# Kernel optimization log

Hardware: AMD Instinct MI355X
Metric: run time of the kernel (lower is better)

## Reference

```python
import jax, jax.numpy as jnp
import numpy as np

FFT_BINS = 513   # win_length//2 + 1
WIN = 1024       # win_length
H = 128          # LSTM hidden size (both blocks)
ENC = 256        # encoder_size
EPS = 1e-7


def _lstm_cell(x, h, c, Wih, Whh, bih, bhh):
    # x: [1, in], h/c: [1, H]; PyTorch gate order i, f, g, o
    g = x @ Wih.T + bih + h @ Whh.T + bhh
    i, f, gg, o = jnp.split(g, 4, axis=-1)
    c2 = jax.nn.sigmoid(f) * c + jax.nn.sigmoid(i) * jnp.tanh(gg)
    h2 = jax.nn.sigmoid(o) * jnp.tanh(c2)
    return h2, c2


def _sep_block(x, states, Wih0, Whh0, bih0, bhh0, Wih1, Whh1, bih1, bhh1, dw, db):
    # x: [1,1,in]; states: [1,1,2*2*H] -> [2(h/c), 2(layers), 1, H]
    st = states.reshape(2, 2, 1, H)
    h0, c0 = st[0], st[1]
    xt = x[:, 0]                                   # [1, in]
    h1, c1 = _lstm_cell(xt, h0[0], c0[0], Wih0, Whh0, bih0, bhh0)
    h2, c2 = _lstm_cell(h1, h0[1], c0[1], Wih1, Whh1, bih1, bhh1)
    mask = jax.nn.sigmoid(h2 @ dw.T + db)[:, None, :]   # [1,1,in]
    out_states = jnp.stack([jnp.stack([h1, h2]), jnp.stack([c1, c2])]).reshape(1, 1, -1)
    return mask, out_states


def setup_inputs() -> dict:
    key = jax.random.key(0)
    ks = jax.random.split(key, 32)
    s = 0.08  # ~ 1/sqrt(H), matching PyTorch LSTM init scale
    def n(i, shape, sc=s):
        return jax.random.normal(ks[i], shape, dtype=jnp.float32) * sc
    inp = {
        "mag": jax.random.uniform(ks[0], (1, 1, FFT_BINS), dtype=jnp.float32),
        "phase": n(1, (1, 1, FFT_BINS), 3.0),
        "in_states1": n(2, (1, 1, 2 * 2 * H), 1.0),
        "in_states2": n(3, (1, 1, 2 * 2 * H), 1.0),
        # sep1 LSTM (input 513)
        "w_ih1_0": n(4, (4 * H, FFT_BINS)), "w_hh1_0": n(5, (4 * H, H)),
        "b_ih1_0": n(6, (4 * H,)), "b_hh1_0": n(7, (4 * H,)),
        "w_ih1_1": n(8, (4 * H, H)), "w_hh1_1": n(9, (4 * H, H)),
        "b_ih1_1": n(10, (4 * H,)), "b_hh1_1": n(11, (4 * H,)),
        "dense1_w": n(12, (FFT_BINS, H)), "dense1_b": n(13, (FFT_BINS,)),
        # encoder 1x1 conv (no bias) + instant layernorm
        "enc_w": n(14, (ENC, WIN)),
        "gamma": jnp.ones((1, 1, ENC), jnp.float32),
        "beta": jnp.zeros((1, 1, ENC), jnp.float32),
        # sep2 LSTM (input 256)
        "w_ih2_0": n(15, (4 * H, ENC)), "w_hh2_0": n(16, (4 * H, H)),
        "b_ih2_0": n(17, (4 * H,)), "b_hh2_0": n(18, (4 * H,)),
        "w_ih2_1": n(19, (4 * H, H)), "w_hh2_1": n(20, (4 * H, H)),
        "b_ih2_1": n(21, (4 * H,)), "b_hh2_1": n(22, (4 * H,)),
        "dense2_w": n(23, (ENC, H)), "dense2_b": n(24, (ENC,)),
        # decoder 1x1 conv (no bias)
        "dec_w": n(25, (WIN, ENC)),
    }
    return inp


def reference(mag, phase, in_states1, in_states2,
              w_ih1_0, w_hh1_0, b_ih1_0, b_hh1_0,
              w_ih1_1, w_hh1_1, b_ih1_1, b_hh1_1,
              dense1_w, dense1_b, enc_w, gamma, beta,
              w_ih2_0, w_hh2_0, b_ih2_0, b_hh2_0,
              w_ih2_1, w_hh2_1, b_ih2_1, b_hh2_1,
              dense2_w, dense2_b, dec_w):
    # Branch 1: magnitude masking in STFT domain
    mask1, out_states1 = _sep_block(mag, in_states1, w_ih1_0, w_hh1_0, b_ih1_0,
                                    b_hh1_0, w_ih1_1, w_hh1_1, b_ih1_1, b_hh1_1,
                                    dense1_w, dense1_b)
    est_mag = mask1 * mag
    s1_stft = est_mag * jnp.exp(1j * phase)          # [1,1,513] complex64
    y1 = jnp.fft.irfft(s1_stft, axis=-1)             # [1,1,1024]
    # encoder 1x1 conv (permute + conv1d(k=1) == matmul over channels)
    enc = jnp.einsum('btw,ew->bte', y1, enc_w)       # [1,1,256]
    # instant layer norm over channels
    mean = jnp.mean(enc, axis=-1, keepdims=True)
    var = jnp.mean(jnp.square(enc - mean), axis=-1, keepdims=True)
    enc_norm = (enc - mean) / jnp.sqrt(var + EPS) * gamma + beta
    # Branch 2: learned-domain masking
    mask2, out_states2 = _sep_block(enc_norm, in_states2, w_ih2_0, w_hh2_0,
                                    b_ih2_0, b_hh2_0, w_ih2_1, w_hh2_1,
                                    b_ih2_1, b_hh2_1, dense2_w, dense2_b)
    est_enc = mask2 * enc
    decoded = jnp.einsum('bte,we->bwt', est_enc, dec_w)  # [1,1024,1]
    return decoded, out_states1, out_states2
```

## Files before the change

### kernel.cpp

```cpp
#include <hip/hip_runtime.h>
#include <hip/hip_bf16.h>


#define HDIM 128
typedef __hip_bfloat16 bf16;

__device__ float G[4608];
#define O_H1A 0
#define O_H2A 128
#define O_C1A 256
#define O_C2A 384
#define O_H1B 512
#define O_H2B 640
#define O_C1B 768
#define O_C2B 896
#define O_XR  1024
#define O_XI  1600
#define O_Y   2176
#define O_ENC 3200
#define O_EST 3456

__device__ __forceinline__ bool is_bf(const void* probe) {
    return (((const unsigned*)probe)[0] & 0xFFFFu) == 0x3F80u;
}
__device__ __forceinline__ float ldin(const void* p, int i, bool bf) {
    return bf ? __bfloat162float(((const bf16*)p)[i]) : ((const float*)p)[i];
}
__device__ __forceinline__ void stout(void* p, int i, float v, bool bf) {
    if (bf) ((bf16*)p)[i] = __float2bfloat16(v);
    else    ((float*)p)[i] = v;
}
__device__ __forceinline__ float wred(float v) {
#pragma unroll
    for (int m = 32; m; m >>= 1) v += __shfl_xor(v, m);
    return v;
}
__device__ __forceinline__ float sigm(float x) { return 1.f / (1.f + expf(-x)); }

template <int LX, bool XINT>
__global__ __launch_bounds__(256) void k_lstm(
    const void* __restrict__ xp, int xoff,
    const void* __restrict__ st, int hoff, int coff,
    const void* __restrict__ Wih, const void* __restrict__ Whh,
    const void* __restrict__ bih, const void* __restrict__ bhh,
    int ho, int co, const void* __restrict__ probe)
{
    const bool bf = is_bf(probe);
    __shared__ float xs[LX];
    __shared__ float hs[HDIM];
    __shared__ float g4[4];
    const int tid = threadIdx.x, lane = tid & 63, wave = tid >> 6;
    const int j = blockIdx.x;
    for (int i = tid; i < LX; i += 256)
        xs[i] = XINT ? G[xoff + i] : ldin(xp, xoff + i, bf);
    for (int i = tid; i < HDIM; i += 256)
        hs[i] = ldin(st, hoff + i, bf);
    __syncthreads();
    const int row = wave * HDIM + j;
    float acc = 0.f;
    for (int k = lane; k < LX; k += 64) acc += ldin(Wih, row * LX + k, bf) * xs[k];
    for (int k = lane; k < HDIM; k += 64) acc += ldin(Whh, row * HDIM + k, bf) * hs[k];
    acc = wred(acc);
    if (lane == 0) g4[wave] = acc + ldin(bih, row, bf) + ldin(bhh, row, bf);
    __syncthreads();
    if (tid == 0) {
        float cin = ldin(st, coff + j, bf);
        float c2 = sigm(g4[1]) * cin + sigm(g4[0]) * tanhf(g4[2]);
        float h2 = sigm(g4[3]) * tanhf(c2);
        G[ho + j] = h2;
        G[co + j] = c2;
    }
}

__global__ __launch_bounds__(256) void k_lstm_ln(
    const void* __restrict__ gamma, const void* __restrict__ beta,
    const void* __restrict__ st,
    const void* __restrict__ Wih, const void* __restrict__ Whh,
    const void* __restrict__ bih, const void* __restrict__ bhh,
    const void* __restrict__ probe)
{
    const bool bf = is_bf(probe);
    __shared__ float xs[256];
    __shared__ float hs[HDIM];
    __shared__ float red[4];
    __shared__ float g4[4];
    const int tid = threadIdx.x, lane = tid & 63, wave = tid >> 6;
    const int j = blockIdx.x;
    float v = G[O_ENC + tid];
    float s = wred(v);
    if (lane == 0) red[wave] = s;
    __syncthreads();
    float mean = (red[0] + red[1] + red[2] + red[3]) * (1.f / 256.f);
    __syncthreads();
    float d = v - mean;
    float s2 = wred(d * d);
    if (lane == 0) red[wave] = s2;
    __syncthreads();
    float var = (red[0] + red[1] + red[2] + red[3]) * (1.f / 256.f);
    float rs = rsqrtf(var + 1e-7f);
    xs[tid] = d * rs * ldin(gamma, tid, bf) + ldin(beta, tid, bf);
    for (int i = tid; i < HDIM; i += 256) hs[i] = ldin(st, i, bf);
    __syncthreads();
    const int row = wave * HDIM + j;
    float acc = 0.f;
    for (int k = lane; k < 256; k += 64) acc += ldin(Wih, row * 256 + k, bf) * xs[k];
    for (int k = lane; k < HDIM; k += 64) acc += ldin(Whh, row * HDIM + k, bf) * hs[k];
    acc = wred(acc);
    if (lane == 0) g4[wave] = acc + ldin(bih, row, bf) + ldin(bhh, row, bf);
    __syncthreads();
    if (tid == 0) {
        float cin = ldin(st, 256 + j, bf);
        float c2 = sigm(g4[1]) * cin + sigm(g4[0]) * tanhf(g4[2]);
        float h2 = sigm(g4[3]) * tanhf(c2);
        G[O_H1B + j] = h2;
        G[O_C1B + j] = c2;
    }
}

__global__ __launch_bounds__(256) void k_mask1(
    const void* __restrict__ dw, const void* __restrict__ db,
    const void* __restrict__ mag, const void* __restrict__ phase,
    void* __restrict__ out, const void* __restrict__ probe)
{
    const bool bf = is_bf(probe);
    __shared__ float hs[HDIM];
    const int tid = threadIdx.x, lane = tid & 63, wave = tid >> 6;
    for (int i = tid; i < HDIM; i += 256) hs[i] = G[O_H2A + i];
    __syncthreads();
    const int g = blockIdx.x * 4 + wave;
    if (g < 513) {
        float acc = 0.f;
        for (int k = lane; k < HDIM; k += 64) acc += ldin(dw, g * HDIM + k, bf) * hs[k];
        acc = wred(acc);
        if (lane == 0) {
            float m = sigm(acc + ldin(db, g, bf));
            float em = m * ldin(mag, g, bf);
            float p = ldin(phase, g, bf);
            float sp, cp;
            sincosf(p, &sp, &cp);
            G[O_XR + g] = em * cp;
            G[O_XI + g] = em * sp;
        }
    }
    if (blockIdx.x == 0) {
        for (int t = tid; t < 512; t += 256) stout(out, 1024 + t, G[t], bf);
    }
}

__global__ __launch_bounds__(256) void k_irfft()
{
    __shared__ float xr[513], xi[513];
    const int tid = threadIdx.x, lane = tid & 63, wave = tid >> 6;
    for (int i = tid; i < 513; i += 256) { xr[i] = G[O_XR + i]; xi[i] = G[O_XI + i]; }
    __syncthreads();
    const int n = blockIdx.x * 4 + wave;
    float acc = 0.f;
    for (int k = lane; k < 513; k += 64) {
        if (k == 0) {
            acc += xr[0];
        } else if (k == 512) {
            acc += (n & 1) ? -xr[512] : xr[512];
        } else {
            int m = (k * n) & 1023;
            float th = (float)m * (6.283185307179586f / 1024.f);
            float sn, cs;
            sincosf(th, &sn, &cs);
            acc += 2.f * (xr[k] * cs - xi[k] * sn);
        }
    }
    acc = wred(acc);
    if (lane == 0) G[O_Y + n] = acc * (1.f / 1024.f);
}

__global__ __launch_bounds__(256) void k_enc(
    const void* __restrict__ ew, const void* __restrict__ probe)
{
    const bool bf = is_bf(probe);
    __shared__ float ys[1024];
    const int tid = threadIdx.x, lane = tid & 63, wave = tid >> 6;
    for (int i = tid; i < 1024; i += 256) ys[i] = G[O_Y + i];
    __syncthreads();
    const int e = blockIdx.x * 4 + wave;
    float acc = 0.f;
    for (int k = lane; k < 1024; k += 64) acc += ldin(ew, e * 1024 + k, bf) * ys[k];
    acc = wred(acc);
    if (lane == 0) G[O_ENC + e] = acc;
}

__global__ __launch_bounds__(256) void k_mask2(
    const void* __restrict__ dw, const void* __restrict__ db,
    void* __restrict__ out, const void* __restrict__ probe)
{
    const bool bf = is_bf(probe);
    __shared__ float hs[HDIM];
    const int tid = threadIdx.x, lane = tid & 63, wave = tid >> 6;
    for (int i = tid; i < HDIM; i += 256) hs[i] = G[O_H2B + i];
    __syncthreads();
    const int e = blockIdx.x * 4 + wave;
    float acc = 0.f;
    for (int k = lane; k < HDIM; k += 64) acc += ldin(dw, e * HDIM + k, bf) * hs[k];
    acc = wred(acc);
    if (lane == 0) {
        float m = sigm(acc + ldin(db, e, bf));
        G[O_EST + e] = m * G[O_ENC + e];
    }
    if (blockIdx.x == 0) {
        for (int t = tid; t < 512; t += 256) stout(out, 1536 + t, G[512 + t], bf);
    }
}

__global__ __launch_bounds__(256) void k_dec(
    const void* __restrict__ dw, void* __restrict__ out, const void* __restrict__ probe)
{
    const bool bf = is_bf(probe);
    __shared__ float es[256];
    const int tid = threadIdx.x, lane = tid & 63, wave = tid >> 6;
    es[tid] = G[O_EST + tid];
    __syncthreads();
    const int w = blockIdx.x * 4 + wave;
    float acc = 0.f;
    for (int k = lane; k < 256; k += 64) acc += ldin(dw, w * 256 + k, bf) * es[k];
    acc = wred(acc);
    if (lane == 0) stout(out, w, acc, bf);
}

extern "C" void kernel_launch(void* const* d_in, const int* in_sizes, int n_in,
                              void* d_out, int out_size, void* d_ws, size_t ws_size,
                              hipStream_t stream)
{
    const void* mag      = d_in[0];
    const void* phase    = d_in[1];
    const void* st1      = d_in[2];
    const void* st2      = d_in[3];
    const void* w_ih1_0  = d_in[4];
    const void* w_hh1_0  = d_in[5];
    const void* b_ih1_0  = d_in[6];
    const void* b_hh1_0  = d_in[7];
    const void* w_ih1_1  = d_in[8];
    const void* w_hh1_1  = d_in[9];
    const void* b_ih1_1  = d_in[10];
    const void* b_hh1_1  = d_in[11];
    const void* dense1_w = d_in[12];
    const void* dense1_b = d_in[13];
    const void* enc_w    = d_in[14];
    const void* gamma    = d_in[15];
    const void* beta     = d_in[16];
    const void* w_ih2_0  = d_in[17];
    const void* w_hh2_0  = d_in[18];
    const void* b_ih2_0  = d_in[19];
    const void* b_hh2_0  = d_in[20];
    const void* w_ih2_1  = d_in[21];
    const void* w_hh2_1  = d_in[22];
    const void* b_ih2_1  = d_in[23];
    const void* b_hh2_1  = d_in[24];
    const void* dense2_w = d_in[25];
    const void* dense2_b = d_in[26];
    const void* dec_w    = d_in[27];

    k_lstm<513, false><<<128, 256, 0, stream>>>(
        mag, 0, st1, 0, 256, w_ih1_0, w_hh1_0, b_ih1_0, b_hh1_0, O_H1A, O_C1A, gamma);
    k_lstm<128, true><<<128, 256, 0, stream>>>(
        nullptr, O_H1A, st1, 128, 384, w_ih1_1, w_hh1_1, b_ih1_1, b_hh1_1, O_H2A, O_C2A, gamma);
    k_mask1<<<129, 256, 0, stream>>>(dense1_w, dense1_b, mag, phase, d_out, gamma);

    k_irfft<<<256, 256, 0, stream>>>();
    k_enc<<<64, 256, 0, stream>>>(enc_w, gamma);

    k_lstm_ln<<<128, 256, 0, stream>>>(
        gamma, beta, st2, w_ih2_0, w_hh2_0, b_ih2_0, b_hh2_0, gamma);
    k_lstm<128, true><<<128, 256, 0, stream>>>(
        nullptr, O_H1B, st2, 128, 384, w_ih2_1, w_hh2_1, b_ih2_1, b_hh2_1, O_H2B, O_C2B, gamma);
    k_mask2<<<64, 256, 0, stream>>>(dense2_w, dense2_b, d_out, gamma);

    k_dec<<<256, 256, 0, stream>>>(dec_w, d_out, gamma);
}
```

Measured before the change: 150.0 us.

## Fuse all nine stage kernels into one cooperative kernel with grid syncs

Replaces the chain of nine dependent kernel launches with a single cooperative kernel of 128 blocks that runs every stage in order, separated by grid.sync barriers. Intermediates still pass through the global G buffer, and stages that used more blocks before now loop so each wave covers several rows. The aim is to remove per-launch overhead and inter-kernel gaps on a latency-bound single-frame workload. In exchange, stages such as the irfft and decoder get less parallelism, and each grid barrier costs time of its own.

```diff
diff --git a/kernel.cpp b/kernel.cpp
--- a/kernel.cpp
+++ b/kernel.cpp
@@ -1,5 +1,8 @@
 #include <hip/hip_runtime.h>
 #include <hip/hip_bf16.h>
+#include <hip/hip_cooperative_groups.h>
+
+namespace cg = cooperative_groups;
 
 
 #define HDIM 128
@@ -37,25 +40,15 @@
 }
 __device__ __forceinline__ float sigm(float x) { return 1.f / (1.f + expf(-x)); }
 
-template <int LX, bool XINT>
-__global__ __launch_bounds__(256) void k_lstm(
-    const void* __restrict__ xp, int xoff,
-    const void* __restrict__ st, int hoff, int coff,
-    const void* __restrict__ Wih, const void* __restrict__ Whh,
-    const void* __restrict__ bih, const void* __restrict__ bhh,
-    int ho, int co, const void* __restrict__ probe)
+struct P { const void* in[28]; void* out; };
+
+__device__ __forceinline__ void lstm_cell(
+    int LX, const float* xs, const float* hs,
+    const void* Wih, const void* Whh, const void* bih, const void* bhh,
+    const void* st, int coff, int ho, int co, bool bf, float* g4)
 {
-    const bool bf = is_bf(probe);
-    __shared__ float xs[LX];
-    __shared__ float hs[HDIM];
-    __shared__ float g4[4];
     const int tid = threadIdx.x, lane = tid & 63, wave = tid >> 6;
     const int j = blockIdx.x;
-    for (int i = tid; i < LX; i += 256)
-        xs[i] = XINT ? G[xoff + i] : ldin(xp, xoff + i, bf);
-    for (int i = tid; i < HDIM; i += 256)
-        hs[i] = ldin(st, hoff + i, bf);
-    __syncthreads();
     const int row = wave * HDIM + j;
     float acc = 0.f;
     for (int k = lane; k < LX; k += 64) acc += ldin(Wih, row * LX + k, bf) * xs[k];
@@ -72,205 +65,140 @@
     }
 }
 
-__global__ __launch_bounds__(256) void k_lstm_ln(
-    const void* __restrict__ gamma, const void* __restrict__ beta,
-    const void* __restrict__ st,
-    const void* __restrict__ Wih, const void* __restrict__ Whh,
-    const void* __restrict__ bih, const void* __restrict__ bhh,
-    const void* __restrict__ probe)
+__global__ __launch_bounds__(256, 1) void dtln_fused(P p)
 {
-    const bool bf = is_bf(probe);
-    __shared__ float xs[256];
-    __shared__ float hs[HDIM];
-    __shared__ float red[4];
-    __shared__ float g4[4];
+    cg::grid_group grid = cg::this_grid();
+    const bool bf = is_bf(p.in[15]);
+    __shared__ float sA[1024];
+    __shared__ float sB[516];
+    __shared__ float sR[8];
     const int tid = threadIdx.x, lane = tid & 63, wave = tid >> 6;
-    const int j = blockIdx.x;
-    float v = G[O_ENC + tid];
-    float s = wred(v);
-    if (lane == 0) red[wave] = s;
-    __syncthreads();
-    float mean = (red[0] + red[1] + red[2] + red[3]) * (1.f / 256.f);
-    __syncthreads();
-    float d = v - mean;
-    float s2 = wred(d * d);
-    if (lane == 0) red[wave] = s2;
-    __syncthreads();
-    float var = (red[0] + red[1] + red[2] + red[3]) * (1.f / 256.f);
-    float rs = rsqrtf(var + 1e-7f);
-    xs[tid] = d * rs * ldin(gamma, tid, bf) + ldin(beta, tid, bf);
-    for (int i = tid; i < HDIM; i += 256) hs[i] = ldin(st, i, bf);
-    __syncthreads();
-    const int row = wave * HDIM + j;
-    float acc = 0.f;
-    for (int k = lane; k < 256; k += 64) acc += ldin(Wih, row * 256 + k, bf) * xs[k];
-    for (int k = lane; k < HDIM; k += 64) acc += ldin(Whh, row * HDIM + k, bf) * hs[k];
-    acc = wred(acc);
-    if (lane == 0) g4[wave] = acc + ldin(bih, row, bf) + ldin(bhh, row, bf);
-    __syncthreads();
-    if (tid == 0) {
-        float cin = ldin(st, 256 + j, bf);
-        float c2 = sigm(g4[1]) * cin + sigm(g4[0]) * tanhf(g4[2]);
-        float h2 = sigm(g4[3]) * tanhf(c2);
-        G[O_H1B + j] = h2;
-        G[O_C1B + j] = c2;
-    }
-}
-
-__global__ __launch_bounds__(256) void k_mask1(
-    const void* __restrict__ dw, const void* __restrict__ db,
-    const void* __restrict__ mag, const void* __restrict__ phase,
-    void* __restrict__ out, const void* __restrict__ probe)
-{
-    const bool bf = is_bf(probe);
-    __shared__ float hs[HDIM];
-    const int tid = threadIdx.x, lane = tid & 63, wave = tid >> 6;
-    for (int i = tid; i < HDIM; i += 256) hs[i] = G[O_H2A + i];
-    __syncthreads();
-    const int g = blockIdx.x * 4 + wave;
-    if (g < 513) {
-        float acc = 0.f;
-        for (int k = lane; k < HDIM; k += 64) acc += ldin(dw, g * HDIM + k, bf) * hs[k];
+    const int b = blockIdx.x;
+    const int gw = b * 4 + wave;
+
+    for (int i = tid; i < 513; i += 256) sA[i] = ldin(p.in[0], i, bf);
+    for (int i = tid; i < HDIM; i += 256) sB[i] = ldin(p.in[2], i, bf);
+    __syncthreads();
+    lstm_cell(513, sA, sB, p.in[4], p.in[5], p.in[6], p.in[7],
+              p.in[2], 256, O_H1A, O_C1A, bf, sR);
+    grid.sync();
+
+    for (int i = tid; i < HDIM; i += 256) { sA[i] = G[O_H1A + i]; sB[i] = ldin(p.in[2], 128 + i, bf); }
+    __syncthreads();
+    lstm_cell(HDIM, sA, sB, p.in[8], p.in[9], p.in[10], p.in[11],
+              p.in[2], 384, O_H2A, O_C2A, bf, sR);
+    grid.sync();
+
+    for (int i = tid; i < HDIM; i += 256) sB[i] = G[O_H2A + i];
+    __syncthreads();
+    for (int g = gw; g < 513; g += 512) {
+        float acc = 0.f;
+        for (int k = lane; k < HDIM; k += 64) acc += ldin(p.in[12], g * HDIM + k, bf) * sB[k];
         acc = wred(acc);
         if (lane == 0) {
-            float m = sigm(acc + ldin(db, g, bf));
-            float em = m * ldin(mag, g, bf);
-            float p = ldin(phase, g, bf);
-            float sp, cp;
-            sincosf(p, &sp, &cp);
+            float m = sigm(acc + ldin(p.in[13], g, bf));
+            float em = m * ldin(p.in[0], g, bf);
+            float ph = ldin(p.in[1], g, bf);
+            float sp, cp; sincosf(ph, &sp, &cp);
             G[O_XR + g] = em * cp;
             G[O_XI + g] = em * sp;
         }
     }
-    if (blockIdx.x == 0) {
-        for (int t = tid; t < 512; t += 256) stout(out, 1024 + t, G[t], bf);
-    }
-}
-
-__global__ __launch_bounds__(256) void k_irfft()
-{
-    __shared__ float xr[513], xi[513];
-    const int tid = threadIdx.x, lane = tid & 63, wave = tid >> 6;
-    for (int i = tid; i < 513; i += 256) { xr[i] = G[O_XR + i]; xi[i] = G[O_XI + i]; }
-    __syncthreads();
-    const int n = blockIdx.x * 4 + wave;
-    float acc = 0.f;
-    for (int k = lane; k < 513; k += 64) {
-        if (k == 0) {
-            acc += xr[0];
-        } else if (k == 512) {
-            acc += (n & 1) ? -xr[512] : xr[512];
-        } else {
-            int m = (k * n) & 1023;
-            float th = (float)m * (6.283185307179586f / 1024.f);
-            float sn, cs;
-            sincosf(th, &sn, &cs);
-            acc += 2.f * (xr[k] * cs - xi[k] * sn);
+    if (b == 0)
+        for (int t = tid; t < 512; t += 256) stout(p.out, 1024 + t, G[t], bf);
+    grid.sync();
+
+    for (int i = tid; i < 513; i += 256) { sA[i] = G[O_XR + i]; sB[i] = G[O_XI + i]; }
+    __syncthreads();
+    for (int n = gw; n < 1024; n += 512) {
+        float acc = 0.f;
+        for (int k = lane; k < 513; k += 64) {
+            if (k == 0) {
+                acc += sA[0];
+            } else if (k == 512) {
+                acc += (n & 1) ? -sA[512] : sA[512];
+            } else {
+                int m = (k * n) & 1023;
+                float th = (float)m * (6.283185307179586f / 1024.f);
+                float sn, cs; sincosf(th, &sn, &cs);
+                acc += 2.f * (sA[k] * cs - sB[k] * sn);
+            }
         }
-    }
-    acc = wred(acc);
-    if (lane == 0) G[O_Y + n] = acc * (1.f / 1024.f);
-}
-
-__global__ __launch_bounds__(256) void k_enc(
-    const void* __restrict__ ew, const void* __restrict__ probe)
-{
-    const bool bf = is_bf(probe);
-    __shared__ float ys[1024];
-    const int tid = threadIdx.x, lane = tid & 63, wave = tid >> 6;
-    for (int i = tid; i < 1024; i += 256) ys[i] = G[O_Y + i];
-    __syncthreads();
-    const int e = blockIdx.x * 4 + wave;
-    float acc = 0.f;
-    for (int k = lane; k < 1024; k += 64) acc += ldin(ew, e * 1024 + k, bf) * ys[k];
-    acc = wred(acc);
-    if (lane == 0) G[O_ENC + e] = acc;
-}
-
-__global__ __launch_bounds__(256) void k_mask2(
-    const void* __restrict__ dw, const void* __restrict__ db,
-    void* __restrict__ out, const void* __restrict__ probe)
-{
-    const bool bf = is_bf(probe);
-    __shared__ float hs[HDIM];
-    const int tid = threadIdx.x, lane = tid & 63, wave = tid >> 6;
-    for (int i = tid; i < HDIM; i += 256) hs[i] = G[O_H2B + i];
-    __syncthreads();
-    const int e = blockIdx.x * 4 + wave;
-    float acc = 0.f;
-    for (int k = lane; k < HDIM; k += 64) acc += ldin(dw, e * HDIM + k, bf) * hs[k];
-    acc = wred(acc);
-    if (lane == 0) {
-        float m = sigm(acc + ldin(db, e, bf));
-        G[O_EST + e] = m * G[O_ENC + e];
-    }
-    if (blockIdx.x == 0) {
-        for (int t = tid; t < 512; t += 256) stout(out, 1536 + t, G[512 + t], bf);
-    }
-}
-
-__global__ __launch_bounds__(256) void k_dec(
-    const void* __restrict__ dw, void* __restrict__ out, const void* __restrict__ probe)
-{
-    const bool bf = is_bf(probe);
-    __shared__ float es[256];
-    const int tid = threadIdx.x, lane = tid & 63, wave = tid >> 6;
-    es[tid] = G[O_EST + tid];
-    __syncthreads();
-    const int w = blockIdx.x * 4 + wave;
-    float acc = 0.f;
-    for (int k = lane; k < 256; k += 64) acc += ldin(dw, w * 256 + k, bf) * es[k];
-    acc = wred(acc);
-    if (lane == 0) stout(out, w, acc, bf);
+        acc = wred(acc);
+        if (lane == 0) G[O_Y + n] = acc * (1.f / 1024.f);
+    }
+    grid.sync();
+
+    for (int i = tid; i < 1024; i += 256) sA[i] = G[O_Y + i];
+    __syncthreads();
+    if (gw < 256) {
+        float acc = 0.f;
+        for (int k = lane; k < 1024; k += 64) acc += ldin(p.in[14], gw * 1024 + k, bf) * sA[k];
+        acc = wred(acc);
+        if (lane == 0) G[O_ENC + gw] = acc;
+    }
+    grid.sync();
+
+    {
+        float v = G[O_ENC + tid];
+        float s = wred(v);
+        if (lane == 0) sR[4 + wave] = s;
+        __syncthreads();
+        float mean = (sR[4] + sR[5] + sR[6] + sR[7]) * (1.f / 256.f);
+        __syncthreads();
+        float d = v - mean;
+        float s2 = wred(d * d);
+        if (lane == 0) sR[4 + wave] = s2;
+        __syncthreads();
+        float var = (sR[4] + sR[5] + sR[6] + sR[7]) * (1.f / 256.f);
+        float rs = rsqrtf(var + 1e-7f);
+        sA[tid] = d * rs * ldin(p.in[15], tid, bf) + ldin(p.in[16], tid, bf);
+        for (int i = tid; i < HDIM; i += 256) sB[i] = ldin(p.in[3], i, bf);
+        __syncthreads();
+        lstm_cell(256, sA, sB, p.in[17], p.in[18], p.in[19], p.in[20],
+                  p.in[3], 256, O_H1B, O_C1B, bf, sR);
+    }
+    grid.sync();
+
+    for (int i = tid; i < HDIM; i += 256) { sA[i] = G[O_H1B + i]; sB[i] = ldin(p.in[3], 128 + i, bf); }
+    __syncthreads();
+    lstm_cell(HDIM, sA, sB, p.in[21], p.in[22], p.in[23], p.in[24],
+              p.in[3], 384, O_H2B, O_C2B, bf, sR);
+    grid.sync();
+
+    for (int i = tid; i < HDIM; i += 256) sB[i] = G[O_H2B + i];
+    __syncthreads();
+    if (gw < 256) {
+        float acc = 0.f;
+        for (int k = lane; k < HDIM; k += 64) acc += ldin(p.in[25], gw * HDIM + k, bf) * sB[k];
+        acc = wred(acc);
+        if (lane == 0) {
+            float m = sigm(acc + ldin(p.in[26], gw, bf));
+            G[O_EST + gw] = m * G[O_ENC + gw];
+        }
+    }
+    if (b == 0)
+        for (int t = tid; t < 512; t += 256) stout(p.out, 1536 + t, G[512 + t], bf);
+    grid.sync();
+
+    for (int i = tid; i < 256; i += 256) sA[i] = G[O_EST + i];
+    __syncthreads();
+    for (int w = gw; w < 1024; w += 512) {
+        float acc = 0.f;
+        for (int k = lane; k < 256; k += 64) acc += ldin(p.in[27], w * 256 + k, bf) * sA[k];
+        acc = wred(acc);
+        if (lane == 0) stout(p.out, w, acc, bf);
+    }
 }
 
 extern "C" void kernel_launch(void* const* d_in, const int* in_sizes, int n_in,
                               void* d_out, int out_size, void* d_ws, size_t ws_size,
                               hipStream_t stream)
 {
-    const void* mag      = d_in[0];
-    const void* phase    = d_in[1];
-    const void* st1      = d_in[2];
-    const void* st2      = d_in[3];
-    const void* w_ih1_0  = d_in[4];
-    const void* w_hh1_0  = d_in[5];
-    const void* b_ih1_0  = d_in[6];
-    const void* b_hh1_0  = d_in[7];
-    const void* w_ih1_1  = d_in[8];
-    const void* w_hh1_1  = d_in[9];
-    const void* b_ih1_1  = d_in[10];
-    const void* b_hh1_1  = d_in[11];
-    const void* dense1_w = d_in[12];
-    const void* dense1_b = d_in[13];
-    const void* enc_w    = d_in[14];
-    const void* gamma    = d_in[15];
-    const void* beta     = d_in[16];
-    const void* w_ih2_0  = d_in[17];
-    const void* w_hh2_0  = d_in[18];
-    const void* b_ih2_0  = d_in[19];
-    const void* b_hh2_0  = d_in[20];
-    const void* w_ih2_1  = d_in[21];
-    const void* w_hh2_1  = d_in[22];
-    const void* b_ih2_1  = d_in[23];
-    const void* b_hh2_1  = d_in[24];
-    const void* dense2_w = d_in[25];
-    const void* dense2_b = d_in[26];
-    const void* dec_w    = d_in[27];
-
-    k_lstm<513, false><<<128, 256, 0, stream>>>(
-        mag, 0, st1, 0, 256, w_ih1_0, w_hh1_0, b_ih1_0, b_hh1_0, O_H1A, O_C1A, gamma);
-    k_lstm<128, true><<<128, 256, 0, stream>>>(
-        nullptr, O_H1A, st1, 128, 384, w_ih1_1, w_hh1_1, b_ih1_1, b_hh1_1, O_H2A, O_C2A, gamma);
-    k_mask1<<<129, 256, 0, stream>>>(dense1_w, dense1_b, mag, phase, d_out, gamma);
-
-    k_irfft<<<256, 256, 0, stream>>>();
-    k_enc<<<64, 256, 0, stream>>>(enc_w, gamma);
-
-    k_lstm_ln<<<128, 256, 0, stream>>>(
-        gamma, beta, st2, w_ih2_0, w_hh2_0, b_ih2_0, b_hh2_0, gamma);
-    k_lstm<128, true><<<128, 256, 0, stream>>>(
-        nullptr, O_H1B, st2, 128, 384, w_ih2_1, w_hh2_1, b_ih2_1, b_hh2_1, O_H2B, O_C2B, gamma);
-    k_mask2<<<64, 256, 0, stream>>>(dense2_w, dense2_b, d_out, gamma);
-
-    k_dec<<<256, 256, 0, stream>>>(dec_w, d_out, gamma);
-}
+    P p;
+    for (int i = 0; i < 28; ++i) p.in[i] = d_in[i];
+    p.out = d_out;
+    void* args[] = { &p };
+    hipLaunchCooperativeKernel((const void*)dtln_fused, dim3(128), dim3(256),
+                               args, 0, stream);
+}
```

After: 296.9 us. 1.98x slower.
